# Optimization experiments

Hardware: AMD Instinct MI355X
Metric: run time of the kernel (lower is better)

## Reference

```python
import jax, jax.numpy as jnp
import numpy as np

B, T, C, H, D = 4, 1024, 1024, 16, 64  # batch, seq, n_embd, heads, head_size


def setup_inputs() -> dict:
    key = jax.random.key(0)
    ks = jax.random.split(key, 6)
    x = jax.random.normal(ks[0], (B, T, C), dtype=jnp.float32)
    s = 0.02
    Wq = jax.random.normal(ks[1], (H, C, D), dtype=jnp.float32) * s
    Wk = jax.random.normal(ks[2], (H, C, D), dtype=jnp.float32) * s
    Wv = jax.random.normal(ks[3], (H, C, D), dtype=jnp.float32) * s
    Wo = jax.random.normal(ks[4], (H * D, C), dtype=jnp.float32) * s
    bo = jnp.zeros((C,), dtype=jnp.float32)
    return {"x": x, "Wq": Wq, "Wk": Wk, "Wv": Wv, "Wo": Wo, "bo": bo}


def reference(x, Wq, Wk, Wv, Wo, bo):
    # per-head projections (bias=False Linears), all heads batched via einsum
    q = jnp.einsum("btc,hcd->bhtd", x, Wq)
    k = jnp.einsum("btc,hcd->bhtd", x, Wk)
    v = jnp.einsum("btc,hcd->bhtd", x, Wv)
    # scaled dot-product scores: [B,H,T,T]
    scale = 1.0 / jnp.sqrt(jnp.asarray(D, dtype=q.dtype))
    scores = jnp.einsum("bhtd,bhsd->bhts", q, k) * scale
    # causal mask (tril), masked_fill with -inf equivalent
    causal = jnp.tril(jnp.ones((T, T), dtype=bool))
    neg = jnp.finfo(scores.dtype).min
    scores = jnp.where(causal[None, None], scores, neg)
    att = jax.nn.softmax(scores, axis=-1)
    # weighted aggregation of values, then concat heads
    out = jnp.einsum("bhts,bhsd->bhtd", att, v)
    out = out.transpose(0, 2, 1, 3).reshape(B, T, H * D)
    # output projection
    return out @ Wo + bo
```

## Files before the change

### kernel.cpp

```cpp
#include <hip/hip_runtime.h>
#include <hip/hip_bf16.h>
#include <stdint.h>


typedef float f32x4 __attribute__((ext_vector_type(4)));
typedef __bf16 bf16x8 __attribute__((ext_vector_type(8)));
typedef __bf16 bf16x4 __attribute__((ext_vector_type(4)));

#define GAS __attribute__((address_space(1)))
#define LAS __attribute__((address_space(3)))

__global__ __launch_bounds__(256) void cast_bf16_kernel(
    const float* __restrict__ in, __bf16* __restrict__ out, int n4) {
  int i = blockIdx.x * 256 + threadIdx.x;
  if (i < n4) {
    float4 f = ((const float4*)in)[i];
    bf16x4 o;
    o[0] = (__bf16)f.x; o[1] = (__bf16)f.y; o[2] = (__bf16)f.z; o[3] = (__bf16)f.w;
    ((bf16x4*)out)[i] = o;
  }
}

__global__ __launch_bounds__(256) void transpose_qkv_kernel(
    const float* __restrict__ Wq, const float* __restrict__ Wk,
    const float* __restrict__ Wv, __bf16* __restrict__ dst_base) {
  __shared__ float tile[64][65];
  int z = blockIdx.z;
  const float* s = (z < 16 ? Wq : (z < 32 ? Wk : Wv)) + (size_t)(z & 15) * 65536;
  __bf16* d = dst_base + (size_t)z * 65536;
  int r0 = blockIdx.x * 64;
  int tx = threadIdx.x & 63, ty = threadIdx.x >> 6;
#pragma unroll
  for (int rr = ty; rr < 64; rr += 4)
    tile[rr][tx] = s[(size_t)(r0 + rr) * 64 + tx];
  __syncthreads();
#pragma unroll
  for (int rr = ty; rr < 64; rr += 4)
    d[(size_t)rr * 1024 + (r0 + tx)] = (__bf16)tile[tx][rr];
}

__global__ __launch_bounds__(256) void transpose_cast_kernel(
    const float* __restrict__ src, __bf16* __restrict__ dst,
    int src_ld, int dst_ld) {
  __shared__ float tile[64][65];
  int r0 = blockIdx.x * 64, c0 = blockIdx.y * 64;
  int tx = threadIdx.x & 63, ty = threadIdx.x >> 6;
#pragma unroll
  for (int rr = ty; rr < 64; rr += 4)
    tile[rr][tx] = src[(size_t)(r0 + rr) * src_ld + (c0 + tx)];
  __syncthreads();
#pragma unroll
  for (int rr = ty; rr < 64; rr += 4)
    dst[(size_t)(c0 + rr) * dst_ld + (r0 + tx)] = (__bf16)tile[tx][rr];
}

template <int MODE>
__global__ __launch_bounds__(256) void gemm_bt_kernel(
    const __bf16* __restrict__ A, const __bf16* __restrict__ BT, int N,
    __bf16* __restrict__ qo, __bf16* __restrict__ ko, __bf16* __restrict__ vo,
    float* __restrict__ Cout, const float* __restrict__ bias) {
  constexpr int K = 1024;
  extern __shared__ __align__(16) char smem_raw[];
  __bf16* Ash = (__bf16*)smem_raw;
  __bf16* Bsh = Ash + 2 * 128 * 32;
  const int tid = threadIdx.x;
  const int wid = tid >> 6, lane = tid & 63;
  const int fr = lane & 15, fq = lane >> 4;
  const int m0 = blockIdx.x * 128, n0 = blockIdx.y * 128;
  const int wr = wid >> 1, wc = wid & 1;
  const int srow = lane >> 2;
  const int scol = (((lane & 3) ^ ((lane >> 3) & 3))) * 8;
  const int swz = ((fq ^ ((fr >> 1) & 3))) << 3;

  f32x4 acc[4][4] = {};

  auto stage = [&](int k0, int buf) {
#pragma unroll
    for (int i = 0; i < 2; ++i) {
      int chunk = wid * 2 + i;
      int row = chunk * 16 + srow;
      const __bf16* gA = A + (size_t)(m0 + row) * K + k0 + scol;
      const __bf16* gB = BT + (size_t)(n0 + row) * K + k0 + scol;
      __builtin_amdgcn_global_load_lds((const GAS void*)gA, (LAS void*)&Ash[buf * 4096 + chunk * 512], 16, 0, 0);
      __builtin_amdgcn_global_load_lds((const GAS void*)gB, (LAS void*)&Bsh[buf * 4096 + chunk * 512], 16, 0, 0);
    }
  };

  stage(0, 0);
  __syncthreads();
  int buf = 0;
  for (int k0 = 0; k0 < K; k0 += 32) {
    if (k0 + 32 < K) stage(k0 + 32, buf ^ 1);
    bf16x8 af[4], bfr[4];
#pragma unroll
    for (int mi = 0; mi < 4; ++mi) {
      int r = wr * 64 + mi * 16 + fr;
      af[mi] = *(const bf16x8*)&Ash[buf * 4096 + r * 32 + swz];
    }
#pragma unroll
    for (int ni = 0; ni < 4; ++ni) {
      int r = wc * 64 + ni * 16 + fr;
      bfr[ni] = *(const bf16x8*)&Bsh[buf * 4096 + r * 32 + swz];
    }
    __builtin_amdgcn_s_setprio(1);
#pragma unroll
    for (int mi = 0; mi < 4; ++mi)
#pragma unroll
      for (int ni = 0; ni < 4; ++ni)
        acc[mi][ni] = __builtin_amdgcn_mfma_f32_16x16x32_bf16(af[mi], bfr[ni], acc[mi][ni], 0, 0, 0);
    __builtin_amdgcn_s_setprio(0);
    __syncthreads();
    buf ^= 1;
  }

  if (MODE == 0 && (n0 >> 10) == 2) {
    __bf16* spill = (__bf16*)smem_raw;
#pragma unroll
    for (int mi = 0; mi < 4; ++mi)
#pragma unroll
      for (int ni = 0; ni < 4; ++ni) {
        int nl = wc * 64 + ni * 16 + fr;
        int ml = wr * 64 + mi * 16 + fq * 4;
        bf16x4 pk;
#pragma unroll
        for (int r = 0; r < 4; ++r) pk[r] = (__bf16)acc[mi][ni][r];
        *(bf16x4*)&spill[nl * 136 + ml] = pk;
      }
    __syncthreads();
    const int b = m0 >> 10, t0 = m0 & 1023;
    const int lrow = lane >> 4, lch = lane & 15;
#pragma unroll
    for (int i = 0; i < 8; ++i) {
      int nl = wid * 32 + i * 4 + lrow;
      bf16x8 v = *(const bf16x8*)&spill[nl * 136 + lch * 8];
      int nn = (n0 & 1023) + nl;
      *(bf16x8*)&vo[(((size_t)b * 16 + (nn >> 6)) * 64 + (nn & 63)) * 1024 + t0 + lch * 8] = v;
    }
    return;
  }

#pragma unroll
  for (int mi = 0; mi < 4; ++mi) {
#pragma unroll
    for (int ni = 0; ni < 4; ++ni) {
      int n = n0 + wc * 64 + ni * 16 + fr;
      int mb = m0 + wr * 64 + mi * 16 + fq * 4;
#pragma unroll
      for (int r = 0; r < 4; ++r) {
        int m = mb + r;
        float val = acc[mi][ni][r];
        if (MODE == 0) {
          int nl = n & 1023;
          int h = nl >> 6, dd = nl & 63;
          int b = m >> 10, t = m & 1023;
          if ((n >> 10) == 0) {
            qo[(((size_t)b * 16 + h) * 1024 + t) * 64 + dd] = (__bf16)(val * 0.125f);
          } else {
            ko[(((size_t)b * 16 + h) * 1024 + t) * 64 + dd] = (__bf16)val;
          }
        } else {
          Cout[(size_t)m * N + n] = val + bias[n];
        }
      }
    }
  }
}

__global__ __launch_bounds__(256) void attn_fwd_kernel(
    const __bf16* __restrict__ Q, const __bf16* __restrict__ Kg,
    const __bf16* __restrict__ Vt, __bf16* __restrict__ O) {
  __shared__ __align__(16) __bf16 Ksh[2][64 * 64];
  __shared__ __align__(16) __bf16 VTs[2][64 * 64];
  __shared__ __align__(16) __bf16 Psh[4][16 * 72];

  const int bid = blockIdx.x;
  const int qt = 15 - (bid >> 6);
  const int bh = bid & 63;
  const int b = bh >> 4, h = bh & 15;
  const size_t base = (size_t)bh * 1024 * 64;
  const int tid = threadIdx.x, wid = tid >> 6, lane = tid & 63;
  const int fr = lane & 15, fq = lane >> 4;
  const int q0 = qt * 64;

  bf16x8 qf[2];
  {
    int qr = q0 + wid * 16 + fr;
    qf[0] = *(const bf16x8*)&Q[base + (size_t)qr * 64 + fq * 8];
    qf[1] = *(const bf16x8*)&Q[base + (size_t)qr * 64 + 32 + fq * 8];
  }
  f32x4 oacc[4] = {};
  float m = -1e30f, l = 0.f;

  const int lrow8 = lane >> 3;
  const int schunk = (lane & 7) ^ lrow8;

  auto stage = [&](int st, int buf) {
    const int s0 = st * 64;
#pragma unroll
    for (int i = 0; i < 2; ++i) {
      int rowbase = i * 32 + wid * 8;
      int row = rowbase + lrow8;
      const __bf16* gK = Kg + base + (size_t)(s0 + row) * 64 + schunk * 8;
      __builtin_amdgcn_global_load_lds((const GAS void*)gK,
          (LAS void*)&Ksh[buf][rowbase * 64], 16, 0, 0);
      const __bf16* gV = Vt + base + (size_t)row * 1024 + s0 + schunk * 8;
      __builtin_amdgcn_global_load_lds((const GAS void*)gV,
          (LAS void*)&VTs[buf][rowbase * 64], 16, 0, 0);
    }
  };

  auto compute = [&](int buf, int s0, bool maskT) {
    f32x4 s[4];
    __builtin_amdgcn_s_setprio(1);
#pragma unroll
    for (int sf = 0; sf < 4; ++sf) {
      int row = sf * 16 + fr, rx = fr & 7;
      bf16x8 kf0 = *(const bf16x8*)&Ksh[buf][row * 64 + ((fq ^ rx) << 3)];
      f32x4 z = {};
      s[sf] = __builtin_amdgcn_mfma_f32_16x16x32_bf16(kf0, qf[0], z, 0, 0, 0);
      bf16x8 kf1 = *(const bf16x8*)&Ksh[buf][row * 64 + (((4 + fq) ^ rx) << 3)];
      s[sf] = __builtin_amdgcn_mfma_f32_16x16x32_bf16(kf1, qf[1], s[sf], 0, 0, 0);
    }
    __builtin_amdgcn_s_setprio(0);

    const int qg = q0 + wid * 16 + fr;
    float sv[4][4];
    float mx = -1e30f;
#pragma unroll
    for (int sf = 0; sf < 4; ++sf)
#pragma unroll
      for (int r = 0; r < 4; ++r) {
        float x = s[sf][r];
        if (maskT) { int sg = s0 + sf * 16 + fq * 4 + r; if (sg > qg) x = -1e30f; }
        sv[sf][r] = x;
        mx = fmaxf(mx, x);
      }
    mx = fmaxf(mx, __shfl_xor(mx, 16));
    mx = fmaxf(mx, __shfl_xor(mx, 32));
    if (__any(mx - m > 8.0f)) {
      float mnew = fmaxf(m, mx);
      float alpha = __expf(m - mnew);
      m = mnew;
      l *= alpha;
      float ar[4];
#pragma unroll
      for (int r = 0; r < 4; ++r) ar[r] = __shfl(alpha, (lane & 48) | (fq * 4 + r));
#pragma unroll
      for (int df = 0; df < 4; ++df)
#pragma unroll
        for (int r = 0; r < 4; ++r) oacc[df][r] *= ar[r];
    }
    float rs = 0.f;
#pragma unroll
    for (int sf = 0; sf < 4; ++sf) {
      bf16x4 pk;
#pragma unroll
      for (int r = 0; r < 4; ++r) {
        float p = __expf(sv[sf][r] - m);
        rs += p;
        pk[r] = (__bf16)p;
      }
      *(bf16x4*)&Psh[wid][fr * 72 + sf * 16 + fq * 4] = pk;
    }
    rs += __shfl_xor(rs, 16);
    rs += __shfl_xor(rs, 32);
    l += rs;

    __builtin_amdgcn_s_setprio(1);
#pragma unroll
    for (int kk = 0; kk < 2; ++kk) {
      bf16x8 pf = *(const bf16x8*)&Psh[wid][fr * 72 + kk * 32 + fq * 8];
#pragma unroll
      for (int df = 0; df < 4; ++df) {
        int row = df * 16 + fr;
        bf16x8 vf = *(const bf16x8*)&VTs[buf][row * 64 + ((((kk << 2) | fq) ^ (fr & 7)) << 3)];
        oacc[df] = __builtin_amdgcn_mfma_f32_16x16x32_bf16(pf, vf, oacc[df], 0, 0, 0);
      }
    }
    __builtin_amdgcn_s_setprio(0);
  };

  stage(0, 0);
  __syncthreads();
  int cur = 0;
  for (int st = 0; st <= qt; ++st) {
    if (st < qt) stage(st + 1, cur ^ 1);
    compute(cur, st * 64, st == qt);
    __syncthreads();
    cur ^= 1;
  }

  float lr[4];
#pragma unroll
  for (int r = 0; r < 4; ++r) lr[r] = __shfl(l, (lane & 48) | (fq * 4 + r));
#pragma unroll
  for (int r = 0; r < 4; ++r) {
    float inv = 1.0f / lr[r];
    int t = q0 + wid * 16 + fq * 4 + r;
    size_t orow = ((size_t)b * 1024 + t) * 1024 + h * 64;
#pragma unroll
    for (int df = 0; df < 4; ++df)
      O[orow + df * 16 + fr] = (__bf16)(oacc[df][r] * inv);
  }
}

extern "C" void kernel_launch(void* const* d_in, const int* in_sizes, int n_in,
                              void* d_out, int out_size, void* d_ws, size_t ws_size,
                              hipStream_t stream) {
  const float* x  = (const float*)d_in[0];
  const float* Wq = (const float*)d_in[1];
  const float* Wk = (const float*)d_in[2];
  const float* Wv = (const float*)d_in[3];
  const float* Wo = (const float*)d_in[4];
  const float* bo = (const float*)d_in[5];
  float* out = (float*)d_out;

  __bf16* xb    = (__bf16*)d_ws;
  __bf16* wqkvT = xb + (size_t)4096 * 1024;
  __bf16* woT   = wqkvT + (size_t)3072 * 1024;
  __bf16* qb    = woT + (size_t)1024 * 1024;
  __bf16* kb    = qb + (size_t)4 * 16 * 1024 * 64;
  __bf16* vtb   = kb + (size_t)4 * 16 * 1024 * 64;
  __bf16* Ob    = vtb + (size_t)4 * 16 * 1024 * 64;

  cast_bf16_kernel<<<4096, 256, 0, stream>>>(x, xb, 4194304 / 4);
  transpose_qkv_kernel<<<dim3(16, 1, 48), 256, 0, stream>>>(Wq, Wk, Wv, wqkvT);
  transpose_cast_kernel<<<dim3(16, 16), 256, 0, stream>>>(Wo, woT, 1024, 1024);

  gemm_bt_kernel<0><<<dim3(32, 24), 256, 34816, stream>>>(xb, wqkvT, 3072, qb, kb, vtb, nullptr, nullptr);

  attn_fwd_kernel<<<1024, 256, 0, stream>>>(qb, kb, vtb, Ob);

  gemm_bt_kernel<1><<<dim3(32, 8), 256, 32768, stream>>>(Ob, woT, 1024,
      nullptr, nullptr, nullptr, out, bo);
}
```

Before: 95.27 us.

## Pass softmax P through lane shuffles instead of LDS; swizzle GEMM block order

The attention kernel now rearranges the P probabilities from the MFMA accumulator layout into the A-operand layout using cross-lane shuffles, so the per-wave LDS P buffer and its store/load round trip go away. The GEMM kernel also remaps its linear block index so that consecutive blocks are spread across groups of eight, which is meant to improve cache locality across compute units. The shuffle path costs several extra shuffle instructions per tile, and the block remap assumes the block count divides evenly by eight.

```diff
diff --git a/kernel.cpp b/kernel.cpp
--- a/kernel.cpp
+++ b/kernel.cpp
@@ -9,6 +9,13 @@
 
 #define GAS __attribute__((address_space(1)))
 #define LAS __attribute__((address_space(3)))
+
+__device__ inline unsigned long long shfl64(unsigned long long v, int src) {
+  int2 a = __builtin_bit_cast(int2, v);
+  a.x = __shfl(a.x, src);
+  a.y = __shfl(a.y, src);
+  return __builtin_bit_cast(unsigned long long, a);
+}
 
 __global__ __launch_bounds__(256) void cast_bf16_kernel(
     const float* __restrict__ in, __bf16* __restrict__ out, int n4) {
@@ -66,7 +73,10 @@
   const int tid = threadIdx.x;
   const int wid = tid >> 6, lane = tid & 63;
   const int fr = lane & 15, fq = lane >> 4;
-  const int m0 = blockIdx.x * 128, n0 = blockIdx.y * 128;
+  const int gx = gridDim.x, nb = gx * gridDim.y;
+  const int orig = blockIdx.y * gx + blockIdx.x;
+  const int nl = (orig & 7) * (nb >> 3) + (orig >> 3);
+  const int m0 = (nl % gx) * 128, n0 = (nl / gx) * 128;
   const int wr = wid >> 1, wc = wid & 1;
   const int srow = lane >> 2;
   const int scol = (((lane & 3) ^ ((lane >> 3) & 3))) * 8;
@@ -119,21 +129,21 @@
     for (int mi = 0; mi < 4; ++mi)
 #pragma unroll
       for (int ni = 0; ni < 4; ++ni) {
-        int nl = wc * 64 + ni * 16 + fr;
+        int nlv = wc * 64 + ni * 16 + fr;
         int ml = wr * 64 + mi * 16 + fq * 4;
         bf16x4 pk;
 #pragma unroll
         for (int r = 0; r < 4; ++r) pk[r] = (__bf16)acc[mi][ni][r];
-        *(bf16x4*)&spill[nl * 136 + ml] = pk;
+        *(bf16x4*)&spill[nlv * 136 + ml] = pk;
       }
     __syncthreads();
     const int b = m0 >> 10, t0 = m0 & 1023;
     const int lrow = lane >> 4, lch = lane & 15;
 #pragma unroll
     for (int i = 0; i < 8; ++i) {
-      int nl = wid * 32 + i * 4 + lrow;
-      bf16x8 v = *(const bf16x8*)&spill[nl * 136 + lch * 8];
-      int nn = (n0 & 1023) + nl;
+      int nlv = wid * 32 + i * 4 + lrow;
+      bf16x8 v = *(const bf16x8*)&spill[nlv * 136 + lch * 8];
+      int nn = (n0 & 1023) + nlv;
       *(bf16x8*)&vo[(((size_t)b * 16 + (nn >> 6)) * 64 + (nn & 63)) * 1024 + t0 + lch * 8] = v;
     }
     return;
@@ -150,8 +160,8 @@
         int m = mb + r;
         float val = acc[mi][ni][r];
         if (MODE == 0) {
-          int nl = n & 1023;
-          int h = nl >> 6, dd = nl & 63;
+          int nlv = n & 1023;
+          int h = nlv >> 6, dd = nlv & 63;
           int b = m >> 10, t = m & 1023;
           if ((n >> 10) == 0) {
             qo[(((size_t)b * 16 + h) * 1024 + t) * 64 + dd] = (__bf16)(val * 0.125f);
@@ -171,7 +181,6 @@
     const __bf16* __restrict__ Vt, __bf16* __restrict__ O) {
   __shared__ __align__(16) __bf16 Ksh[2][64 * 64];
   __shared__ __align__(16) __bf16 VTs[2][64 * 64];
-  __shared__ __align__(16) __bf16 Psh[4][16 * 72];
 
   const int bid = blockIdx.x;
   const int qt = 15 - (bid >> 6);
@@ -251,6 +260,7 @@
         for (int r = 0; r < 4; ++r) oacc[df][r] *= ar[r];
     }
     float rs = 0.f;
+    unsigned long long J[4];
 #pragma unroll
     for (int sf = 0; sf < 4; ++sf) {
       bf16x4 pk;
@@ -260,24 +270,33 @@
         rs += p;
         pk[r] = (__bf16)p;
       }
-      *(bf16x4*)&Psh[wid][fr * 72 + sf * 16 + fq * 4] = pk;
+      J[sf] = __builtin_bit_cast(unsigned long long, pk);
     }
     rs += __shfl_xor(rs, 16);
     rs += __shfl_xor(rs, 32);
     l += rs;
 
-    __builtin_amdgcn_s_setprio(1);
+    const int srcA = (lane & 15) | ((lane & 16) << 1);
+    const bool hi = (lane & 32) != 0;
 #pragma unroll
     for (int kk = 0; kk < 2; ++kk) {
-      bf16x8 pf = *(const bf16x8*)&Psh[wid][fr * 72 + kk * 32 + fq * 8];
+      unsigned long long xA = shfl64(J[2 * kk], srcA);
+      unsigned long long yA = shfl64(J[2 * kk + 1], srcA);
+      unsigned long long xB = shfl64(J[2 * kk], srcA + 16);
+      unsigned long long yB = shfl64(J[2 * kk + 1], srcA + 16);
+      union { unsigned long long u[2]; bf16x8 v8; } U;
+      U.u[0] = hi ? yA : xA;
+      U.u[1] = hi ? yB : xB;
+      bf16x8 pf = U.v8;
+      __builtin_amdgcn_s_setprio(1);
 #pragma unroll
       for (int df = 0; df < 4; ++df) {
         int row = df * 16 + fr;
         bf16x8 vf = *(const bf16x8*)&VTs[buf][row * 64 + ((((kk << 2) | fq) ^ (fr & 7)) << 3)];
         oacc[df] = __builtin_amdgcn_mfma_f32_16x16x32_bf16(pf, vf, oacc[df], 0, 0, 0);
       }
-    }
-    __builtin_amdgcn_s_setprio(0);
+      __builtin_amdgcn_s_setprio(0);
+    }
   };
 
   stage(0, 0);
```

Measured after the change: 100.4 us. 1.05x slower.
